# Kernel optimization log

Hardware: AMD Instinct MI355X
Metric: run time of the kernel (lower is better)

Reference implementation:

```python
import jax, jax.numpy as jnp
import numpy as np
import math

NUM_HEADS = 8
BN_EPS = 1e-5
L2_EPS = 1e-6


def _pe2d(C, Hs, Ws, dtype=jnp.float32):
    """Fixed 2D sinusoidal positional encoding, shape (1, C, H, W).
    First C/2 channels encode the x (width) position, last C/2 the y (height)
    position, each as interleaved sin/cos with standard 10000-base frequencies."""
    d = C // 2
    div = jnp.exp(jnp.arange(0, d, 2, dtype=dtype) * (-math.log(10000.0) / d))  # (d/2,)

    def emb(n):
        pos = jnp.arange(n, dtype=dtype)[:, None] * div[None, :]          # (n, d/2)
        return jnp.stack([jnp.sin(pos), jnp.cos(pos)], axis=-1).reshape(n, d)  # (n, d)

    ew = emb(Ws).T  # (d, W)
    eh = emb(Hs).T  # (d, H)
    pe = jnp.concatenate([
        jnp.broadcast_to(ew[:, None, :], (d, Hs, Ws)),   # x-position channels
        jnp.broadcast_to(eh[:, :, None], (d, Hs, Ws)),   # y-position channels
    ], axis=0)
    return pe[None]  # (1, C, H, W)


def _l2n(t):
    # L2 norm over the FULL channel dim (axis=1), per spatial token, as in the source
    return t / jnp.sqrt(jnp.sum(t * t, axis=1, keepdims=True) + L2_EPS)


def setup_inputs() -> dict:
    key = jax.random.key(0)
    ks = jax.random.split(key, 9)
    B, C, Hs, Ws = 2, 256, 48, 48
    scale = 1.0 / math.sqrt(C)
    return {
        "x": jax.random.normal(ks[0], (B, C, Hs, Ws), jnp.float32),
        "gamma": 1.0 + 0.1 * jax.random.normal(ks[1], (C,), jnp.float32),
        "beta": 0.1 * jax.random.normal(ks[2], (C,), jnp.float32),
        "running_mean": 0.1 * jax.random.normal(ks[3], (C,), jnp.float32),
        "running_var": jax.random.uniform(ks[4], (C,), jnp.float32, 0.5, 1.5),
        "v_w": scale * jax.random.normal(ks[5], (C, C), jnp.float32),
        "z_w": scale * jax.random.normal(ks[6], (C, C), jnp.float32),
        "q_w": scale * jax.random.normal(ks[7], (C, C), jnp.float32),
        "o_w": scale * jax.random.normal(ks[8], (C, C), jnp.float32),
    }


def reference(x, gamma, beta, running_mean, running_var, v_w, z_w, q_w, o_w):
    B, C, Hs, Ws = x.shape
    h = NUM_HEADS
    dh = C // h
    M = Hs * Ws

    # BatchNorm2d, inference mode
    inv = gamma / jnp.sqrt(running_var + BN_EPS)
    xn = x * inv[None, :, None, None] + (beta - running_mean * inv)[None, :, None, None]

    # 1x1 convs (bias-free) == channel matmuls
    v = jnp.einsum('oc,bchw->bohw', v_w, xn)
    z = jnp.einsum('oc,bchw->bohw', z_w, xn)
    q = jnp.einsum('oc,bchw->bohw', q_w, xn)

    r = _pe2d(C, Hs, Ws, x.dtype)            # (1, C, H, W)
    zr = _l2n(z) + jnp.broadcast_to(_l2n(r), z.shape)

    vh = v.reshape(B, h, dh, M)
    zrh = zr.reshape(B, h, dh, M)
    qh = q.reshape(B, h, dh, M)

    logits = jnp.einsum('bhcm,bhcn->bhmn', vh, zrh) / math.sqrt(dh)
    A = jax.nn.softmax(logits, axis=-1)      # (B, h, M, M)
    y = jnp.einsum('bhmn,bhcn->bhcm', A, qh)

    y = y.reshape(B, C, Hs, Ws)
    return jnp.einsum('oc,bchw->bohw', o_w, y)
```

## Files before the change

### kernel.cpp

```cpp
#include <hip/hip_runtime.h>
#include <hip/hip_bf16.h>
#include <math.h>

namespace {
constexpr int kC  = 256;
constexpr int kW  = 48;
constexpr int kM  = 2304;
constexpr int kB  = 2;
constexpr int kDH = 32;
constexpr int kH  = 8;
constexpr int kNT = kM / 32;
}

typedef float  f32x4   __attribute__((ext_vector_type(4)));
typedef float  f32x16  __attribute__((ext_vector_type(16)));
typedef __bf16 bf16x8  __attribute__((ext_vector_type(8)));

__device__ __forceinline__ f32x4 mfma16(bf16x8 a, bf16x8 b, f32x4 c) {
    return __builtin_amdgcn_mfma_f32_16x16x32_bf16(a, b, c, 0, 0, 0);
}
__device__ __forceinline__ f32x16 mfma32(bf16x8 a, bf16x8 b, f32x16 c) {
    return __builtin_amdgcn_mfma_f32_32x32x16_bf16(a, b, c, 0, 0, 0);
}
__device__ __forceinline__ float hexp2(float x) { return __builtin_amdgcn_exp2f(x); }


__global__ __launch_bounds__(256) void setup_kernel(
    const float* __restrict__ gamma, const float* __restrict__ beta,
    const float* __restrict__ rmean, const float* __restrict__ rvar,
    const float* __restrict__ w0, const float* __restrict__ w1,
    const float* __restrict__ w2, const float* __restrict__ w3,
    float* __restrict__ bninv, float* __restrict__ bnshift, float* __restrict__ PEt,
    __hip_bfloat16* __restrict__ o0, __hip_bfloat16* __restrict__ o1,
    __hip_bfloat16* __restrict__ o2, __hip_bfloat16* __restrict__ o3) {
    int bid = blockIdx.x, t = threadIdx.x;
    if (bid < 256) {
        int wi = bid >> 6;
        const float* w = wi == 0 ? w0 : wi == 1 ? w1 : wi == 2 ? w2 : w3;
        __hip_bfloat16* o = wi == 0 ? o0 : wi == 1 ? o1 : wi == 2 ? o2 : o3;
        int idx = ((bid & 63) * 256 + t) * 4;
        float4 v = *reinterpret_cast<const float4*>(w + idx);
        o[idx]     = __float2bfloat16(v.x);
        o[idx + 1] = __float2bfloat16(v.y);
        o[idx + 2] = __float2bfloat16(v.z);
        o[idx + 3] = __float2bfloat16(v.w);
    } else if (bid == 256) {
        float iv = gamma[t] / sqrtf(rvar[t] + 1e-5f);
        bninv[t] = iv;
        bnshift[t] = beta[t] - rmean[t] * iv;
    } else {
        int pos = bid - 257;
        int cc = (t < 128) ? t : (t - 128);
        float dv = __expf((float)(cc & ~1) * (float)(-9.210340371976184 / 128.0));
        float pd = (float)pos * dv;
        float rv = (t & 1) ? cosf(pd) : sinf(pd);
        const float RINV = 1.0f / sqrtf(128.0f + 1e-6f);
        PEt[pos * 256 + t] = rv * RINV;
    }
}

__global__ __launch_bounds__(256) void xnt_kernel(const float* __restrict__ x,
                                                  const float* __restrict__ bninv,
                                                  const float* __restrict__ bnshift,
                                                  __hip_bfloat16* __restrict__ Xnt) {
    __shared__ float T[64][65];
    int t = threadIdx.x;
    int m0 = blockIdx.x * 64, c0 = blockIdx.y * 64, b = blockIdx.z;
    int ml = t & 63;
    #pragma unroll
    for (int i = 0; i < 16; i++) {
        int c = (t >> 6) + i * 4;
        T[c][ml] = x[(size_t)(b * kC + c0 + c) * kM + m0 + ml] * bninv[c0 + c] + bnshift[c0 + c];
    }
    __syncthreads();
    int mr = t >> 2, cseg = (t & 3) * 16;
    __hip_bfloat16 v[16];
    #pragma unroll
    for (int j = 0; j < 16; j++) v[j] = __float2bfloat16(T[cseg + j][mr]);
    __hip_bfloat16* dst = Xnt + (size_t)(b * kM + m0 + mr) * kC + c0 + cseg;
    *reinterpret_cast<bf16x8*>(dst)     = *reinterpret_cast<bf16x8*>(&v[0]);
    *reinterpret_cast<bf16x8*>(dst + 8) = *reinterpret_cast<bf16x8*>(&v[8]);
}

__global__ __launch_bounds__(64) void conv_gemm(const __hip_bfloat16* __restrict__ Xnt,
                                                const __hip_bfloat16* __restrict__ Wv,
                                                const __hip_bfloat16* __restrict__ Wz,
                                                const __hip_bfloat16* __restrict__ Wq,
                                                __hip_bfloat16* __restrict__ Vt,
                                                __hip_bfloat16* __restrict__ Zb16,
                                                __hip_bfloat16* __restrict__ Qtt) {
    int t = threadIdx.x, li = t & 15, g = t >> 4;
    int m0 = blockIdx.x * 16, o0 = blockIdx.y * 64;
    int b = blockIdx.z;

    bf16x8 a[8];
    const __hip_bfloat16* ap = Xnt + (size_t)(b * kM + m0 + li) * kC + g * 8;
    #pragma unroll
    for (int kb = 0; kb < 8; kb++) a[kb] = *reinterpret_cast<const bf16x8*>(ap + kb * 32);

    const int mt = m0 >> 5;
    const int mmb = m0 & 31;

    {
        f32x4 acc[4] = {{0,0,0,0},{0,0,0,0},{0,0,0,0},{0,0,0,0}};
        const __hip_bfloat16* wp = Wv + g * 8;
        #pragma unroll
        for (int kb = 0; kb < 8; kb++)
            #pragma unroll
            for (int ot = 0; ot < 4; ot++) {
                bf16x8 bw = *reinterpret_cast<const bf16x8*>(wp + (size_t)(o0 + ot * 16 + li) * kC + kb * 32);
                acc[ot] = mfma16(a[kb], bw, acc[ot]);
            }
        const float SCALE2 = 0.25501988169885635f;
        #pragma unroll
        for (int ot = 0; ot < 4; ot++) {
            int o = o0 + ot * 16 + li, hh = o >> 5, cc = o & 31;
            __hip_bfloat16* base = Vt + (((size_t)(b * kH + hh) * kNT + mt) * 32) * 32 + cc;
            #pragma unroll
            for (int r = 0; r < 4; r++)
                base[(mmb + 4 * g + r) * 32] = __float2bfloat16(acc[ot][r] * SCALE2);
        }
    }
    {
        f32x4 acc[4] = {{0,0,0,0},{0,0,0,0},{0,0,0,0},{0,0,0,0}};
        const __hip_bfloat16* wp = Wz + g * 8;
        #pragma unroll
        for (int kb = 0; kb < 8; kb++)
            #pragma unroll
            for (int ot = 0; ot < 4; ot++) {
                bf16x8 bw = *reinterpret_cast<const bf16x8*>(wp + (size_t)(o0 + ot * 16 + li) * kC + kb * 32);
                acc[ot] = mfma16(a[kb], bw, acc[ot]);
            }
        #pragma unroll
        for (int ot = 0; ot < 4; ot++)
            #pragma unroll
            for (int r = 0; r < 4; r++)
                Zb16[(size_t)(b * kM + m0 + 4 * g + r) * kC + o0 + ot * 16 + li] = __float2bfloat16(acc[ot][r]);
    }
    {
        f32x4 acc[4] = {{0,0,0,0},{0,0,0,0},{0,0,0,0},{0,0,0,0}};
        const __hip_bfloat16* wp = Wq + g * 8;
        #pragma unroll
        for (int kb = 0; kb < 8; kb++)
            #pragma unroll
            for (int ot = 0; ot < 4; ot++) {
                bf16x8 bw = *reinterpret_cast<const bf16x8*>(wp + (size_t)(o0 + ot * 16 + li) * kC + kb * 32);
                acc[ot] = mfma16(a[kb], bw, acc[ot]);
            }
        #pragma unroll
        for (int ot = 0; ot < 4; ot++) {
            int o = o0 + ot * 16 + li, hh = o >> 5, d = o & 31;
            __hip_bfloat16* base = Qtt + (((size_t)(b * kH + hh) * kNT + mt) * 32 + d) * 32 + mmb + 4 * g;
            *reinterpret_cast<__hip_bfloat162*>(base) =
                __float22bfloat162_rn(make_float2(acc[ot][0], acc[ot][1]));
            *reinterpret_cast<__hip_bfloat162*>(base + 2) =
                __float22bfloat162_rn(make_float2(acc[ot][2], acc[ot][3]));
        }
    }
}

__global__ __launch_bounds__(256) void zr_kernel(const __hip_bfloat16* __restrict__ Z,
                                                 const float* __restrict__ PEt,
                                                 __hip_bfloat16* __restrict__ ZRt) {
    int t = threadIdx.x;
    int bm = blockIdx.x * 4 + (t >> 6);
    int lane = t & 63;
    int m = bm % kM, b = bm / kM;
    union { uint2 u; __hip_bfloat16 h[4]; } zu;
    zu.u = *reinterpret_cast<const uint2*>(Z + (size_t)bm * kC + lane * 4);
    float z[4];
    #pragma unroll
    for (int j = 0; j < 4; j++) z[j] = __bfloat162float(zu.h[j]);
    float ss = (z[0]*z[0] + z[1]*z[1]) + (z[2]*z[2] + z[3]*z[3]);
    #pragma unroll
    for (int k = 32; k >= 1; k >>= 1) ss += __shfl_xor(ss, k);
    float zinv = 1.0f / sqrtf(ss + 1e-6f);
    int pos = (lane < 32) ? (m % kW) : (m / kW);
    f32x4 pe = *reinterpret_cast<const f32x4*>(PEt + pos * 256 + lane * 4);
    union { uint2 u; __hip_bfloat16 h[4]; } ou;
    #pragma unroll
    for (int j = 0; j < 4; j++) ou.h[j] = __float2bfloat16(z[j] * zinv + pe[j]);
    int hh = lane >> 3, cc = (lane * 4) & 31;
    *reinterpret_cast<uint2*>(
        ZRt + (((size_t)(b * kH + hh) * kNT + (m >> 5)) * 32 + (m & 31)) * 32 + cc) = ou.u;
}

__global__ __launch_bounds__(512) void flash_attn_fused(
    const __hip_bfloat16* __restrict__ Vt,
    const __hip_bfloat16* __restrict__ ZRt,
    const __hip_bfloat16* __restrict__ Qtt,
    __hip_bfloat16* __restrict__ Y16)
{
    __shared__ float Aw[8][32 * 36];
    __shared__ float Ls[8][64];
    const int t = threadIdx.x;
    const int w = t >> 6, lane = t & 63;
    const int c = lane & 31, hi = lane >> 5;
    const int blk = blockIdx.x;
    const int bh = blk & 15, pair = blk >> 4;
    const int b = bh >> 3, h = bh & 7;
    const f32x16 zero16 = {0,0,0,0,0,0,0,0,0,0,0,0,0,0,0,0};

    const int lo = c * 32 + hi * 8;
    const size_t hb = (size_t)bh * kNT;

    bf16x8 vf[2][2];
    #pragma unroll
    for (int mt = 0; mt < 2; mt++) {
        const __hip_bfloat16* vb = Vt + (hb + pair * 2 + mt) * 1024 + lo;
        vf[mt][0] = *reinterpret_cast<const bf16x8*>(vb);
        vf[mt][1] = *reinterpret_cast<const bf16x8*>(vb + 16);
    }

    const __hip_bfloat16* zb = ZRt + (hb + w * 9) * 1024 + lo;
    const __hip_bfloat16* qb = Qtt + (hb + w * 9) * 1024 + lo;

    f32x16 acc[2] = {zero16, zero16};
    float lsum[2] = {0.f, 0.f};

    bf16x8 za0 = *reinterpret_cast<const bf16x8*>(zb);
    bf16x8 za1 = *reinterpret_cast<const bf16x8*>(zb + 16);
    bf16x8 qa0 = *reinterpret_cast<const bf16x8*>(qb);
    bf16x8 qa1 = *reinterpret_cast<const bf16x8*>(qb + 16);

    for (int it = 0; it < 9; ++it) {
        const int nx = (it < 8) ? (it + 1) * 1024 : 0;

        bf16x8 za0n = *reinterpret_cast<const bf16x8*>(zb + nx);
        bf16x8 za1n = *reinterpret_cast<const bf16x8*>(zb + nx + 16);
        bf16x8 qa0n = *reinterpret_cast<const bf16x8*>(qb + nx);
        bf16x8 qa1n = *reinterpret_cast<const bf16x8*>(qb + nx + 16);

        #pragma unroll
        for (int mt = 0; mt < 2; mt++) {
            f32x16 st = mfma32(za0, vf[mt][0], zero16);
            st = mfma32(za1, vf[mt][1], st);

            float p[16];
            #pragma unroll
            for (int r = 0; r < 16; r++) p[r] = hexp2(st[r]);
            float s01 = (p[0] + p[1]) + (p[2] + p[3]);
            float s23 = (p[4] + p[5]) + (p[6] + p[7]);
            float s45 = (p[8] + p[9]) + (p[10] + p[11]);
            float s67 = (p[12] + p[13]) + (p[14] + p[15]);
            lsum[mt] += (s01 + s23) + (s45 + s67);

            #pragma unroll
            for (int kk = 0; kk < 2; kk++) {
                __hip_bfloat162 xw0 = __float22bfloat162_rn(make_float2(p[8*kk+0], p[8*kk+1]));
                __hip_bfloat162 xw1 = __float22bfloat162_rn(make_float2(p[8*kk+2], p[8*kk+3]));
                __hip_bfloat162 yw0 = __float22bfloat162_rn(make_float2(p[8*kk+4], p[8*kk+5]));
                __hip_bfloat162 yw1 = __float22bfloat162_rn(make_float2(p[8*kk+6], p[8*kk+7]));
                unsigned x0 = *reinterpret_cast<unsigned*>(&xw0);
                unsigned x1 = *reinterpret_cast<unsigned*>(&xw1);
                unsigned y0 = *reinterpret_cast<unsigned*>(&yw0);
                unsigned y1 = *reinterpret_cast<unsigned*>(&yw1);
                asm("v_permlane32_swap_b32 %0, %1" : "+v"(x0), "+v"(y0));
                asm("v_permlane32_swap_b32 %0, %1" : "+v"(x1), "+v"(y1));
                union { unsigned u[4]; bf16x8 v; } bf;
                bf.u[0] = x0; bf.u[1] = x1; bf.u[2] = y0; bf.u[3] = y1;
                acc[mt] = mfma32(kk == 0 ? qa0 : qa1, bf.v, acc[mt]);
            }
        }

        za0 = za0n; za1 = za1n; qa0 = qa0n; qa1 = qa1n;
    }

    #pragma unroll
    for (int mt = 0; mt < 2; mt++) {
        #pragma unroll
        for (int r = 0; r < 16; r++) {
            int dh = (r & 3) + 8 * (r >> 2) + 4 * hi;
            Aw[w][c * 36 + dh] = acc[mt][r];
        }
        Ls[w][lane] = lsum[mt];
        __syncthreads();

        if (t < 256) {
            const int m = t & 31, dh0 = (t >> 5) * 4;
            float L = 0.f;
            #pragma unroll
            for (int w2 = 0; w2 < 8; w2++) L += Ls[w2][m] + Ls[w2][m + 32];
            f32x4 s4 = {0.f, 0.f, 0.f, 0.f};
            #pragma unroll
            for (int w2 = 0; w2 < 8; w2++)
                s4 = s4 + *reinterpret_cast<const f32x4*>(&Aw[w2][m * 36 + dh0]);
            float inv = 1.0f / L;
            union { uint2 u2; __hip_bfloat162 h2[2]; } o;
            o.h2[0] = __float22bfloat162_rn(make_float2(s4[0] * inv, s4[1] * inv));
            o.h2[1] = __float22bfloat162_rn(make_float2(s4[2] * inv, s4[3] * inv));
            *reinterpret_cast<uint2*>(
                Y16 + (size_t)(b * kM + (pair * 2 + mt) * 32 + m) * kC + h * kDH + dh0) = o.u2;
        }
        __syncthreads();
    }
}

__global__ __launch_bounds__(64) void conv_out_gemm(const __hip_bfloat16* __restrict__ Y16,
                                                    const __hip_bfloat16* __restrict__ Wo,
                                                    float* __restrict__ out) {
    int t = threadIdx.x, li = t & 15, g = t >> 4;
    int m0 = blockIdx.x * 16, o0 = blockIdx.y * 64, b = blockIdx.z;

    bf16x8 a[8];
    const __hip_bfloat16* ap = Y16 + (size_t)(b * kM + m0 + li) * kC + g * 8;
    #pragma unroll
    for (int kb = 0; kb < 8; kb++) a[kb] = *reinterpret_cast<const bf16x8*>(ap + kb * 32);

    f32x4 acc[4] = {{0,0,0,0},{0,0,0,0},{0,0,0,0},{0,0,0,0}};
    const __hip_bfloat16* wp = Wo + g * 8;
    #pragma unroll
    for (int kb = 0; kb < 8; kb++) {
        #pragma unroll
        for (int ot = 0; ot < 4; ot++) {
            bf16x8 bw = *reinterpret_cast<const bf16x8*>(wp + (size_t)(o0 + ot * 16 + li) * kC + kb * 32);
            acc[ot] = mfma16(a[kb], bw, acc[ot]);
        }
    }
    #pragma unroll
    for (int ot = 0; ot < 4; ot++) {
        int o = o0 + ot * 16 + li;
        *reinterpret_cast<f32x4*>(out + (size_t)(b * kC + o) * kM + m0 + 4 * g) = acc[ot];
    }
}

extern "C" void kernel_launch(void* const* d_in, const int* in_sizes, int n_in,
                              void* d_out, int out_size, void* d_ws, size_t ws_size,
                              hipStream_t stream) {
    const float* x     = (const float*)d_in[0];
    const float* gamma = (const float*)d_in[1];
    const float* beta  = (const float*)d_in[2];
    const float* rmean = (const float*)d_in[3];
    const float* rvar  = (const float*)d_in[4];
    const float* v_w   = (const float*)d_in[5];
    const float* z_w   = (const float*)d_in[6];
    const float* q_w   = (const float*)d_in[7];
    const float* o_w   = (const float*)d_in[8];
    float* out = (float*)d_out;

    char* wsb = (char*)d_ws;
    const size_t BMC = (size_t)kB * kM * kC;
    float* bninv   = (float*)wsb;
    float* bnshift = (float*)(wsb + 1024);
    float* PEt     = (float*)(wsb + 4096);
    __hip_bfloat16* Wv16 = (__hip_bfloat16*)(wsb + 53248);
    __hip_bfloat16* Wz16 = Wv16 + 65536;
    __hip_bfloat16* Wq16 = Wz16 + 65536;
    __hip_bfloat16* Wo16 = Wq16 + 65536;
    __hip_bfloat16* Xnt  = Wo16 + 65536;
    __hip_bfloat16* Vt   = Xnt + BMC;
    __hip_bfloat16* Zb16 = Vt + BMC;
    __hip_bfloat16* ZRt  = Zb16 + BMC;
    __hip_bfloat16* Qtt  = ZRt + BMC;
    __hip_bfloat16* Y16  = Qtt + BMC;

    setup_kernel<<<dim3(305), dim3(256), 0, stream>>>(
        gamma, beta, rmean, rvar, v_w, z_w, q_w, o_w,
        bninv, bnshift, PEt, Wv16, Wz16, Wq16, Wo16);
    xnt_kernel<<<dim3(kM / 64, kC / 64, kB), dim3(256), 0, stream>>>(x, bninv, bnshift, Xnt);
    conv_gemm<<<dim3(kM / 16, kC / 64, kB), dim3(64), 0, stream>>>(
        Xnt, Wv16, Wz16, Wq16, Vt, Zb16, Qtt);
    zr_kernel<<<dim3(kB * kM / 4), dim3(256), 0, stream>>>(Zb16, PEt, ZRt);
    flash_attn_fused<<<dim3((kNT / 2) * kH * kB), dim3(512), 0, stream>>>(Vt, ZRt, Qtt, Y16);
    conv_out_gemm<<<dim3(kM / 16, kC / 64, kB), dim3(64), 0, stream>>>(Y16, Wo16, out);
}
```

Measured before the change: 67.42 us.

## Fuse Z L2-normalisation and positional encoding into the conv GEMM kernel

The conv GEMM now uses 256-thread blocks in which four waves cover all 256 output channels for a 16-token tile. The Z projection result is kept in shared memory and normalised in-block, then the positional encoding is added and ZR is written directly. This removes the separate zr_kernel launch and the bf16 Z round trip through global memory. In exchange the grid is smaller and there is an extra shared-memory stage and barrier.

```diff
diff --git a/kernel.cpp b/kernel.cpp
--- a/kernel.cpp
+++ b/kernel.cpp
@@ -82,16 +82,21 @@
     *reinterpret_cast<bf16x8*>(dst + 8) = *reinterpret_cast<bf16x8*>(&v[8]);
 }
 
-__global__ __launch_bounds__(64) void conv_gemm(const __hip_bfloat16* __restrict__ Xnt,
-                                                const __hip_bfloat16* __restrict__ Wv,
-                                                const __hip_bfloat16* __restrict__ Wz,
-                                                const __hip_bfloat16* __restrict__ Wq,
-                                                __hip_bfloat16* __restrict__ Vt,
-                                                __hip_bfloat16* __restrict__ Zb16,
-                                                __hip_bfloat16* __restrict__ Qtt) {
-    int t = threadIdx.x, li = t & 15, g = t >> 4;
-    int m0 = blockIdx.x * 16, o0 = blockIdx.y * 64;
-    int b = blockIdx.z;
+__global__ __launch_bounds__(256) void conv_gemm(const __hip_bfloat16* __restrict__ Xnt,
+                                                 const __hip_bfloat16* __restrict__ Wv,
+                                                 const __hip_bfloat16* __restrict__ Wz,
+                                                 const __hip_bfloat16* __restrict__ Wq,
+                                                 const float* __restrict__ PEt,
+                                                 __hip_bfloat16* __restrict__ Vt,
+                                                 __hip_bfloat16* __restrict__ Qtt,
+                                                 __hip_bfloat16* __restrict__ ZRt) {
+    __shared__ float Zs[16][260];
+    int t = threadIdx.x;
+    int wv = t >> 6, lane = t & 63;
+    int li = lane & 15, g = lane >> 4;
+    int m0 = blockIdx.x * 16;
+    int b = blockIdx.y;
+    int o0 = wv * 64;
 
     bf16x8 a[8];
     const __hip_bfloat16* ap = Xnt + (size_t)(b * kM + m0 + li) * kC + g * 8;
@@ -120,22 +125,6 @@
             for (int r = 0; r < 4; r++)
                 base[(mmb + 4 * g + r) * 32] = __float2bfloat16(acc[ot][r] * SCALE2);
         }
-    }
-    {
-        f32x4 acc[4] = {{0,0,0,0},{0,0,0,0},{0,0,0,0},{0,0,0,0}};
-        const __hip_bfloat16* wp = Wz + g * 8;
-        #pragma unroll
-        for (int kb = 0; kb < 8; kb++)
-            #pragma unroll
-            for (int ot = 0; ot < 4; ot++) {
-                bf16x8 bw = *reinterpret_cast<const bf16x8*>(wp + (size_t)(o0 + ot * 16 + li) * kC + kb * 32);
-                acc[ot] = mfma16(a[kb], bw, acc[ot]);
-            }
-        #pragma unroll
-        for (int ot = 0; ot < 4; ot++)
-            #pragma unroll
-            for (int r = 0; r < 4; r++)
-                Zb16[(size_t)(b * kM + m0 + 4 * g + r) * kC + o0 + ot * 16 + li] = __float2bfloat16(acc[ot][r]);
     }
     {
         f32x4 acc[4] = {{0,0,0,0},{0,0,0,0},{0,0,0,0},{0,0,0,0}};
@@ -157,32 +146,49 @@
                 __float22bfloat162_rn(make_float2(acc[ot][2], acc[ot][3]));
         }
     }
-}
-
-__global__ __launch_bounds__(256) void zr_kernel(const __hip_bfloat16* __restrict__ Z,
-                                                 const float* __restrict__ PEt,
-                                                 __hip_bfloat16* __restrict__ ZRt) {
-    int t = threadIdx.x;
-    int bm = blockIdx.x * 4 + (t >> 6);
-    int lane = t & 63;
-    int m = bm % kM, b = bm / kM;
-    union { uint2 u; __hip_bfloat16 h[4]; } zu;
-    zu.u = *reinterpret_cast<const uint2*>(Z + (size_t)bm * kC + lane * 4);
-    float z[4];
-    #pragma unroll
-    for (int j = 0; j < 4; j++) z[j] = __bfloat162float(zu.h[j]);
-    float ss = (z[0]*z[0] + z[1]*z[1]) + (z[2]*z[2] + z[3]*z[3]);
-    #pragma unroll
-    for (int k = 32; k >= 1; k >>= 1) ss += __shfl_xor(ss, k);
-    float zinv = 1.0f / sqrtf(ss + 1e-6f);
-    int pos = (lane < 32) ? (m % kW) : (m / kW);
-    f32x4 pe = *reinterpret_cast<const f32x4*>(PEt + pos * 256 + lane * 4);
-    union { uint2 u; __hip_bfloat16 h[4]; } ou;
-    #pragma unroll
-    for (int j = 0; j < 4; j++) ou.h[j] = __float2bfloat16(z[j] * zinv + pe[j]);
-    int hh = lane >> 3, cc = (lane * 4) & 31;
-    *reinterpret_cast<uint2*>(
-        ZRt + (((size_t)(b * kH + hh) * kNT + (m >> 5)) * 32 + (m & 31)) * 32 + cc) = ou.u;
+    {
+        f32x4 acc[4] = {{0,0,0,0},{0,0,0,0},{0,0,0,0},{0,0,0,0}};
+        const __hip_bfloat16* wp = Wz + g * 8;
+        #pragma unroll
+        for (int kb = 0; kb < 8; kb++)
+            #pragma unroll
+            for (int ot = 0; ot < 4; ot++) {
+                bf16x8 bw = *reinterpret_cast<const bf16x8*>(wp + (size_t)(o0 + ot * 16 + li) * kC + kb * 32);
+                acc[ot] = mfma16(a[kb], bw, acc[ot]);
+            }
+        #pragma unroll
+        for (int ot = 0; ot < 4; ot++)
+            #pragma unroll
+            for (int r = 0; r < 4; r++)
+                Zs[4 * g + r][o0 + ot * 16 + li] = acc[ot][r];
+    }
+    __syncthreads();
+
+    {
+        const int r = t >> 4, j = t & 15;
+        float v0[16];
+        #pragma unroll
+        for (int jj = 0; jj < 16; jj++) v0[jj] = Zs[r][j * 16 + jj];
+        float s = 0.f;
+        #pragma unroll
+        for (int jj = 0; jj < 16; jj++) s += v0[jj] * v0[jj];
+        s += __shfl_xor(s, 1);
+        s += __shfl_xor(s, 2);
+        s += __shfl_xor(s, 4);
+        s += __shfl_xor(s, 8);
+        float zinv = 1.0f / sqrtf(s + 1e-6f);
+        const int m = m0 + r;
+        const int pos = (j < 8) ? (m % kW) : (m / kW);
+        const float* pe = PEt + pos * 256 + j * 16;
+        __hip_bfloat16 outv[16];
+        #pragma unroll
+        for (int jj = 0; jj < 16; jj++)
+            outv[jj] = __float2bfloat16(v0[jj] * zinv + pe[jj]);
+        const int hh = j >> 1, cc = (j & 1) * 16;
+        __hip_bfloat16* dst = ZRt + (((size_t)(b * kH + hh) * kNT + (m >> 5)) * 32 + (m & 31)) * 32 + cc;
+        *reinterpret_cast<bf16x8*>(dst)     = *reinterpret_cast<bf16x8*>(&outv[0]);
+        *reinterpret_cast<bf16x8*>(dst + 8) = *reinterpret_cast<bf16x8*>(&outv[8]);
+    }
 }
 
 __global__ __launch_bounds__(512) void flash_attn_fused(
@@ -349,8 +355,7 @@
     __hip_bfloat16* Wo16 = Wq16 + 65536;
     __hip_bfloat16* Xnt  = Wo16 + 65536;
     __hip_bfloat16* Vt   = Xnt + BMC;
-    __hip_bfloat16* Zb16 = Vt + BMC;
-    __hip_bfloat16* ZRt  = Zb16 + BMC;
+    __hip_bfloat16* ZRt  = Vt + BMC;
     __hip_bfloat16* Qtt  = ZRt + BMC;
     __hip_bfloat16* Y16  = Qtt + BMC;
 
@@ -358,9 +363,8 @@
         gamma, beta, rmean, rvar, v_w, z_w, q_w, o_w,
         bninv, bnshift, PEt, Wv16, Wz16, Wq16, Wo16);
     xnt_kernel<<<dim3(kM / 64, kC / 64, kB), dim3(256), 0, stream>>>(x, bninv, bnshift, Xnt);
-    conv_gemm<<<dim3(kM / 16, kC / 64, kB), dim3(64), 0, stream>>>(
-        Xnt, Wv16, Wz16, Wq16, Vt, Zb16, Qtt);
-    zr_kernel<<<dim3(kB * kM / 4), dim3(256), 0, stream>>>(Zb16, PEt, ZRt);
+    conv_gemm<<<dim3(kM / 16, kB), dim3(256), 0, stream>>>(
+        Xnt, Wv16, Wz16, Wq16, PEt, Vt, Qtt, ZRt);
     flash_attn_fused<<<dim3((kNT / 2) * kH * kB), dim3(512), 0, stream>>>(Vt, ZRt, Qtt, Y16);
     conv_out_gemm<<<dim3(kM / 16, kC / 64, kB), dim3(64), 0, stream>>>(Y16, Wo16, out);
 }
```

Result: slower. 72.90 us (+8.1%).
